# Optimization experiments

Hardware: AMD Instinct MI355X
Metric: run time of the kernel (lower is better)

The kernel has to match this reference:

```python
import jax, jax.numpy as jnp
import numpy as np
from jax import lax

K, N = 256, 65536

def setup_inputs() -> dict:
    key = jax.random.key(0)
    k1, k2, k3 = jax.random.split(key, 3)
    # obs: non-negative event counts [K, N]
    obs = jax.random.uniform(k1, (K, N), dtype=jnp.float32) * 4.0
    # Beta ~ U(1, 3) [K]
    Beta = 1.0 + 2.0 * jax.random.uniform(k2, (K,), dtype=jnp.float32)
    # Alpha ~ U(0, 0.01) [K, K]
    Alpha = 0.01 * jax.random.uniform(k3, (K, K), dtype=jnp.float32)
    return {"obs": obs, "Beta": Beta, "Alpha": Alpha}

def reference(obs, Beta, Alpha):
    # obs: [K, N], Beta: [K], Alpha: [K, K]
    Kk, Nn = obs.shape
    Mu0 = obs.mean(axis=1) / 10.0 + 0.01            # [K] background rate
    decay = jnp.exp(-Beta)                          # [K]

    # Exponential kernel sum S[t] = sum_{tp<t} obs[:,tp] * Beta * exp(-(t-tp)*Beta)
    # admits recursion H[t] = exp(-Beta) * (H[t-1] + obs[:, t-1]), S[t] = Beta * H[t]
    def step(h, o_prev):
        h_new = decay * (h + o_prev)
        return h_new, h_new

    _, H = lax.scan(step, jnp.zeros((Kk,), obs.dtype), obs[:, :Nn - 1].T)  # [N-1, K]
    S = H * Beta                                    # [N-1, K]
    # lam1[:, t] = softplus(Alpha @ S[t]) for t >= 1; lam1[:, 0] = 0 (by original code)
    lam = jax.nn.softplus(jnp.einsum('jk,tk->tj', Alpha, S))  # [N-1, K]
    lams1 = jnp.concatenate([jnp.zeros((Kk, 1), obs.dtype), lam.T], axis=1)  # [K, N]
    lams0 = jnp.broadcast_to(Mu0[:, None], (Kk, Nn))          # [K, N]

    Nloglams = obs * jnp.log(lams0 + lams1 + 1e-5)
    loglik = (Nloglams - lams0 - lams1).sum()
    return loglik, lams0, lams1
```

## Files before the change

### kernel.cpp

```cpp
#include <hip/hip_runtime.h>
#include <math.h>

#define KK 256
#define NN 65536
#define TT 128
#define TPAD 264
#define NB (NN / TT)

typedef __bf16 bf16x8 __attribute__((ext_vector_type(8)));
typedef float f32x4 __attribute__((ext_vector_type(4)));

__global__ __launch_bounds__(256) void alpha_kernel(const float* __restrict__ Alpha,
                                                    __bf16* __restrict__ AlphaB,
                                                    float* __restrict__ out) {
  const int i = blockIdx.x * 256 + threadIdx.x;
  AlphaB[i] = (__bf16)Alpha[i];
  if (i == 0) out[0] = 0.f;
}

__global__ __launch_bounds__(512, 4) void main_kernel(const float* __restrict__ obs,
                                                      const float* __restrict__ Beta,
                                                      const __bf16* __restrict__ AlphaB,
                                                      float* __restrict__ out,
                                                      float* __restrict__ P) {
  __shared__ __bf16 Slds[TT][TPAD];
  const int tid = threadIdx.x;
  const int bid = blockIdx.x;
  const int tb = ((bid & 7) << 6) | (bid >> 3);
  const int t0 = tb * TT;

  {
    const int ell = tid & 7;
    const int krow0 = tid >> 3;
    for (int it = 0; it < 4; ++it) {
      const int k = it * 64 + krow0;
      const float beta = Beta[k];
      const float d = expf(-beta);
      const float d2 = d * d, d4 = d2 * d2, d8 = d4 * d4;
      float dl = 1.f;
      if (ell & 1) dl *= d;
      if (ell & 2) dl *= d2;
      if (ell & 4) dl *= d4;
      const float* row = obs + (size_t)k * NN;
      float Hc = 0.f;
      if (t0 > 0) {
#pragma unroll
        for (int rnd = 0; rnd < 2; ++rnd) {
          const float u = row[t0 - 16 + rnd * 8 + ell];
          float X = u, y;
          y = __shfl_up(X, 1, 8); X += (ell >= 1 ? d  * y : 0.f);
          y = __shfl_up(X, 2, 8); X += (ell >= 2 ? d2 * y : 0.f);
          y = __shfl_up(X, 4, 8); X += (ell >= 4 ? d4 * y : 0.f);
          const float I7 = __shfl(X, 7, 8);
          Hc = d8 * Hc + d * I7;
        }
      }
      float rsum = 0.f;
#pragma unroll
      for (int rnd = 0; rnd < 16; ++rnd) {
        const int base = 8 * rnd;
        const float u = row[t0 + base + ell];
        rsum += u;
        float X = u, y;
        y = __shfl_up(X, 1, 8); X += (ell >= 1 ? d  * y : 0.f);
        y = __shfl_up(X, 2, 8); X += (ell >= 2 ? d2 * y : 0.f);
        y = __shfl_up(X, 4, 8); X += (ell >= 4 ? d4 * y : 0.f);
        const float Ip = __shfl_up(X, 1, 8);
        const float H = dl * Hc + (ell >= 1 ? d * Ip : 0.f);
        Slds[base + ell][k] = (__bf16)(beta * H);
        const float I7 = __shfl(X, 7, 8);
        Hc = d8 * Hc + d * I7;
      }
      rsum += __shfl_down(rsum, 1, 8);
      rsum += __shfl_down(rsum, 2, 8);
      rsum += __shfl_down(rsum, 4, 8);
      if (ell == 0) P[(size_t)tb * KK + k] = rsum;
    }
  }
  __syncthreads();

  const int wave = tid >> 6;
  const int wj = wave & 3, wc = wave >> 2;
  const int lane = tid & 63;
  const int lquad = lane >> 4;
  const int l16 = lane & 15;

  f32x4 acc[4][4];
#pragma unroll
  for (int a = 0; a < 4; ++a)
#pragma unroll
    for (int b = 0; b < 4; ++b) acc[a][b] = (f32x4){0.f, 0.f, 0.f, 0.f};

  const __bf16* Abase = AlphaB + (size_t)(wj * 64 + l16) * KK + lquad * 8;
  for (int k0 = 0; k0 < KK; k0 += 32) {
    bf16x8 afrag[4], bfrag[4];
#pragma unroll
    for (int js = 0; js < 4; ++js)
      afrag[js] = *(const bf16x8*)(Abase + (size_t)js * 16 * KK + k0);
#pragma unroll
    for (int ts = 0; ts < 4; ++ts)
      bfrag[ts] = *(const bf16x8*)&Slds[wc * 64 + ts * 16 + l16][k0 + lquad * 8];
#pragma unroll
    for (int js = 0; js < 4; ++js)
#pragma unroll
      for (int ts = 0; ts < 4; ++ts)
        acc[js][ts] = __builtin_amdgcn_mfma_f32_16x16x32_bf16(
            afrag[js], bfrag[ts], acc[js][ts], 0, 0, 0);
  }

  float* lams1 = out + 1 + (size_t)KK * NN;
  const int tcol = t0 + wc * 64;
#pragma unroll
  for (int js = 0; js < 4; ++js) {
#pragma unroll
    for (int r = 0; r < 4; ++r) {
      const int j = wj * 64 + js * 16 + lquad * 4 + r;
      const size_t rowoff = (size_t)j * NN + tcol + l16;
#pragma unroll
      for (int ts = 0; ts < 4; ++ts) {
        float v = acc[js][ts][r];
        float lam = v + __logf(1.f + __expf(-v));
        if (tcol + ts * 16 + l16 == 0) lam = 0.f;
        lams1[rowoff + ts * 16] = lam;
      }
    }
  }
}

__global__ __launch_bounds__(512) void loglik_kernel(const float* __restrict__ obs,
                                                     const float* __restrict__ P,
                                                     float* __restrict__ out) {
  const int j = blockIdx.x;
  const int tid = threadIdx.x;

  float s = P[(size_t)tid * KK + j];
  __shared__ float red[512];
  red[tid] = s;
  __syncthreads();
  for (int off = 256; off > 0; off >>= 1) {
    if (tid < off) red[tid] += red[tid + off];
    __syncthreads();
  }
  const float m = red[0] * (1.0f / NN) * 0.1f + 0.01f;

  const float* orow = obs + (size_t)j * NN;
  float* l0row = out + 1 + (size_t)j * NN;
  float* l1row = l0row + (size_t)KK * NN;
  float partial = 0.f;
#pragma unroll 8
  for (int i = 0; i < NN / 512; ++i) {
    const int t = tid + i * 512;
    const float l1 = l1row[t];
    const float o = orow[t];
    l0row[t] = m;
    partial += o * __logf(m + l1 + 1e-5f) - m - l1;
  }

#pragma unroll
  for (int off = 32; off > 0; off >>= 1)
    partial += __shfl_down(partial, off, 64);
  __syncthreads();
  if ((tid & 63) == 0) red[tid >> 6] = partial;
  __syncthreads();
  if (tid == 0) {
    float t = 0.f;
#pragma unroll
    for (int w = 0; w < 8; ++w) t += red[w];
    atomicAdd(out, t);
  }
}

extern "C" void kernel_launch(void* const* d_in, const int* in_sizes, int n_in,
                              void* d_out, int out_size, void* d_ws, size_t ws_size,
                              hipStream_t stream) {
  const float* obs   = (const float*)d_in[0];
  const float* Beta  = (const float*)d_in[1];
  const float* Alpha = (const float*)d_in[2];
  float* out = (float*)d_out;

  __bf16* AlphaB = (__bf16*)d_ws;
  float* P = (float*)(AlphaB + (size_t)KK * KK);

  hipLaunchKernelGGL(alpha_kernel, dim3(KK), dim3(256), 0, stream, Alpha, AlphaB, out);
  hipLaunchKernelGGL(main_kernel, dim3(NB), dim3(512), 0, stream,
                     obs, Beta, AlphaB, out, P);
  hipLaunchKernelGGL(loglik_kernel, dim3(KK), dim3(512), 0, stream, obs, P, out);
}
```

Baseline: 228.5 us.

## Fuse log-likelihood into GEMM epilogue and precompute Mu0 in a prep pass

A prep kernel now computes the per-row background rate Mu0 (a full read of obs) and also converts Alpha to bf16. The main kernel's epilogue then computes the log-likelihood term from the freshly computed lams1 and atomically accumulates it, so lams1 no longer has to be re-read from global memory. A separate lightweight kernel writes the broadcast lams0 with vectorized stores. This removes the second pass over lams1 and obs, at the cost of an extra obs read in the prep kernel and strided, partially uncoalesced obs loads in the epilogue.

```diff
diff --git a/kernel.cpp b/kernel.cpp
--- a/kernel.cpp
+++ b/kernel.cpp
@@ -10,24 +10,47 @@
 typedef __bf16 bf16x8 __attribute__((ext_vector_type(8)));
 typedef float f32x4 __attribute__((ext_vector_type(4)));
 
-__global__ __launch_bounds__(256) void alpha_kernel(const float* __restrict__ Alpha,
-                                                    __bf16* __restrict__ AlphaB,
-                                                    float* __restrict__ out) {
-  const int i = blockIdx.x * 256 + threadIdx.x;
-  AlphaB[i] = (__bf16)Alpha[i];
-  if (i == 0) out[0] = 0.f;
+__global__ __launch_bounds__(512) void prep_kernel(const float* __restrict__ obs,
+                                                   const float* __restrict__ Alpha,
+                                                   float* __restrict__ mu0,
+                                                   __bf16* __restrict__ AlphaB,
+                                                   float* __restrict__ out) {
+  const int j = blockIdx.x;
+  const int tid = threadIdx.x;
+  if (tid < KK) AlphaB[(size_t)j * KK + tid] = (__bf16)Alpha[(size_t)j * KK + tid];
+  const float4* p = (const float4*)(obs + (size_t)j * NN) + tid;
+  float s = 0.f;
+#pragma unroll
+  for (int i = 0; i < 32; ++i) {
+    float4 v = p[i * 512];
+    s += (v.x + v.y) + (v.z + v.w);
+  }
+  __shared__ float red[512];
+  red[tid] = s;
+  __syncthreads();
+  for (int off = 256; off > 0; off >>= 1) {
+    if (tid < off) red[tid] += red[tid + off];
+    __syncthreads();
+  }
+  if (tid == 0) {
+    mu0[j] = red[0] * (1.0f / NN) * 0.1f + 0.01f;
+    if (j == 0) out[0] = 0.f;
+  }
 }
 
 __global__ __launch_bounds__(512, 4) void main_kernel(const float* __restrict__ obs,
                                                       const float* __restrict__ Beta,
+                                                      const float* __restrict__ mu0,
                                                       const __bf16* __restrict__ AlphaB,
-                                                      float* __restrict__ out,
-                                                      float* __restrict__ P) {
+                                                      float* __restrict__ out) {
   __shared__ __bf16 Slds[TT][TPAD];
+  __shared__ float mu0s[KK];
   const int tid = threadIdx.x;
   const int bid = blockIdx.x;
   const int tb = ((bid & 7) << 6) | (bid >> 3);
   const int t0 = tb * TT;
+
+  if (tid < KK) mu0s[tid] = mu0[tid];
 
   {
     const int ell = tid & 7;
@@ -55,12 +78,10 @@
           Hc = d8 * Hc + d * I7;
         }
       }
-      float rsum = 0.f;
 #pragma unroll
       for (int rnd = 0; rnd < 16; ++rnd) {
         const int base = 8 * rnd;
         const float u = row[t0 + base + ell];
-        rsum += u;
         float X = u, y;
         y = __shfl_up(X, 1, 8); X += (ell >= 1 ? d  * y : 0.f);
         y = __shfl_up(X, 2, 8); X += (ell >= 2 ? d2 * y : 0.f);
@@ -71,10 +92,6 @@
         const float I7 = __shfl(X, 7, 8);
         Hc = d8 * Hc + d * I7;
       }
-      rsum += __shfl_down(rsum, 1, 8);
-      rsum += __shfl_down(rsum, 2, 8);
-      rsum += __shfl_down(rsum, 4, 8);
-      if (ell == 0) P[(size_t)tb * KK + k] = rsum;
     }
   }
   __syncthreads();
@@ -108,6 +125,7 @@
             afrag[js], bfrag[ts], acc[js][ts], 0, 0, 0);
   }
 
+  float partial = 0.f;
   float* lams1 = out + 1 + (size_t)KK * NN;
   const int tcol = t0 + wc * 64;
 #pragma unroll
@@ -115,6 +133,7 @@
 #pragma unroll
     for (int r = 0; r < 4; ++r) {
       const int j = wj * 64 + js * 16 + lquad * 4 + r;
+      const float m = mu0s[j];
       const size_t rowoff = (size_t)j * NN + tcol + l16;
 #pragma unroll
       for (int ts = 0; ts < 4; ++ts) {
@@ -122,45 +141,18 @@
         float lam = v + __logf(1.f + __expf(-v));
         if (tcol + ts * 16 + l16 == 0) lam = 0.f;
         lams1[rowoff + ts * 16] = lam;
+        const float o = obs[rowoff + ts * 16];
+        partial += o * __logf(m + lam + 1e-5f) - m - lam;
       }
     }
-  }
-}
-
-__global__ __launch_bounds__(512) void loglik_kernel(const float* __restrict__ obs,
-                                                     const float* __restrict__ P,
-                                                     float* __restrict__ out) {
-  const int j = blockIdx.x;
-  const int tid = threadIdx.x;
-
-  float s = P[(size_t)tid * KK + j];
-  __shared__ float red[512];
-  red[tid] = s;
-  __syncthreads();
-  for (int off = 256; off > 0; off >>= 1) {
-    if (tid < off) red[tid] += red[tid + off];
-    __syncthreads();
-  }
-  const float m = red[0] * (1.0f / NN) * 0.1f + 0.01f;
-
-  const float* orow = obs + (size_t)j * NN;
-  float* l0row = out + 1 + (size_t)j * NN;
-  float* l1row = l0row + (size_t)KK * NN;
-  float partial = 0.f;
-#pragma unroll 8
-  for (int i = 0; i < NN / 512; ++i) {
-    const int t = tid + i * 512;
-    const float l1 = l1row[t];
-    const float o = orow[t];
-    l0row[t] = m;
-    partial += o * __logf(m + l1 + 1e-5f) - m - l1;
   }
 
 #pragma unroll
   for (int off = 32; off > 0; off >>= 1)
     partial += __shfl_down(partial, off, 64);
   __syncthreads();
-  if ((tid & 63) == 0) red[tid >> 6] = partial;
+  float* red = (float*)&Slds[0][0];
+  if (lane == 0) red[wave] = partial;
   __syncthreads();
   if (tid == 0) {
     float t = 0.f;
@@ -168,6 +160,19 @@
     for (int w = 0; w < 8; ++w) t += red[w];
     atomicAdd(out, t);
   }
+}
+
+__global__ __launch_bounds__(512) void lams0_kernel(const float* __restrict__ mu0,
+                                                    float* __restrict__ out) {
+  const int j = blockIdx.x;
+  const int tid = threadIdx.x;
+  const float m = mu0[j];
+  float* row0 = out + 1 + (size_t)j * NN;
+  if (tid < 3) row0[tid] = m;
+  if (tid == 3) row0[NN - 1] = m;
+  f32x4* p4 = (f32x4*)(row0 + 3);
+  const f32x4 mv = {m, m, m, m};
+  for (int i = tid; i < (NN - 4) / 4; i += 512) p4[i] = mv;
 }
 
 extern "C" void kernel_launch(void* const* d_in, const int* in_sizes, int n_in,
@@ -179,10 +184,11 @@
   float* out = (float*)d_out;
 
   __bf16* AlphaB = (__bf16*)d_ws;
-  float* P = (float*)(AlphaB + (size_t)KK * KK);
+  float* mu0 = (float*)(AlphaB + (size_t)KK * KK);
 
-  hipLaunchKernelGGL(alpha_kernel, dim3(KK), dim3(256), 0, stream, Alpha, AlphaB, out);
+  hipLaunchKernelGGL(prep_kernel, dim3(KK), dim3(512), 0, stream, obs, Alpha,
+                     mu0, AlphaB, out);
   hipLaunchKernelGGL(main_kernel, dim3(NB), dim3(512), 0, stream,
-                     obs, Beta, AlphaB, out, P);
-  hipLaunchKernelGGL(loglik_kernel, dim3(KK), dim3(512), 0, stream, obs, P, out);
+                     obs, Beta, mu0, AlphaB, out);
+  hipLaunchKernelGGL(lams0_kernel, dim3(KK), dim3(512), 0, stream, mu0, out);
 }
```

Result: slower. 240.4 us (+5.2%).

## Double time tile, stage lams1 through LDS for coalesced vector stores

Applied to the files above, without the earlier changes.

Doubles the time tile to 256 steps with 1024-thread blocks, halving the number of blocks and their scan warm-up prefixes. The MFMA results are written through shared memory (reusing the S buffer) in two halves so each wave can emit contiguous 16-byte stores along rows of lams1, replacing the scattered 4-byte column stores. The per-block row-sum partials are stored transposed so the loglik kernel can read them contiguously. The trade-offs are extra barriers, fewer resident waves, and LDS traffic for the staging step.

```diff
diff --git a/kernel.cpp b/kernel.cpp
--- a/kernel.cpp
+++ b/kernel.cpp
@@ -3,8 +3,9 @@
 
 #define KK 256
 #define NN 65536
-#define TT 128
+#define TT 256
 #define TPAD 264
+#define CP 260
 #define NB (NN / TT)
 
 typedef __bf16 bf16x8 __attribute__((ext_vector_type(8)));
@@ -18,22 +19,22 @@
   if (i == 0) out[0] = 0.f;
 }
 
-__global__ __launch_bounds__(512, 4) void main_kernel(const float* __restrict__ obs,
-                                                      const float* __restrict__ Beta,
-                                                      const __bf16* __restrict__ AlphaB,
-                                                      float* __restrict__ out,
-                                                      float* __restrict__ P) {
-  __shared__ __bf16 Slds[TT][TPAD];
+__global__ __launch_bounds__(1024, 4) void main_kernel(const float* __restrict__ obs,
+                                                       const float* __restrict__ Beta,
+                                                       const __bf16* __restrict__ AlphaB,
+                                                       float* __restrict__ out,
+                                                       float* __restrict__ P) {
+  __shared__ __align__(16) __bf16 Slds[TT][TPAD];
   const int tid = threadIdx.x;
   const int bid = blockIdx.x;
-  const int tb = ((bid & 7) << 6) | (bid >> 3);
+  const int tb = ((bid & 7) << 5) | (bid >> 3);
   const int t0 = tb * TT;
 
   {
     const int ell = tid & 7;
     const int krow0 = tid >> 3;
-    for (int it = 0; it < 4; ++it) {
-      const int k = it * 64 + krow0;
+    for (int it = 0; it < 2; ++it) {
+      const int k = it * 128 + krow0;
       const float beta = Beta[k];
       const float d = expf(-beta);
       const float d2 = d * d, d4 = d2 * d2, d8 = d4 * d4;
@@ -57,7 +58,7 @@
       }
       float rsum = 0.f;
 #pragma unroll
-      for (int rnd = 0; rnd < 16; ++rnd) {
+      for (int rnd = 0; rnd < 32; ++rnd) {
         const int base = 8 * rnd;
         const float u = row[t0 + base + ell];
         rsum += u;
@@ -74,7 +75,7 @@
       rsum += __shfl_down(rsum, 1, 8);
       rsum += __shfl_down(rsum, 2, 8);
       rsum += __shfl_down(rsum, 4, 8);
-      if (ell == 0) P[(size_t)tb * KK + k] = rsum;
+      if (ell == 0) P[(size_t)k * NB + tb] = rsum;
     }
   }
   __syncthreads();
@@ -108,21 +109,35 @@
             afrag[js], bfrag[ts], acc[js][ts], 0, 0, 0);
   }
 
+  float* Cl = (float*)&Slds[0][0];
   float* lams1 = out + 1 + (size_t)KK * NN;
-  const int tcol = t0 + wc * 64;
-#pragma unroll
-  for (int js = 0; js < 4; ++js) {
-#pragma unroll
-    for (int r = 0; r < 4; ++r) {
-      const int j = wj * 64 + js * 16 + lquad * 4 + r;
-      const size_t rowoff = (size_t)j * NN + tcol + l16;
-#pragma unroll
-      for (int ts = 0; ts < 4; ++ts) {
-        float v = acc[js][ts][r];
-        float lam = v + __logf(1.f + __expf(-v));
-        if (tcol + ts * 16 + l16 == 0) lam = 0.f;
-        lams1[rowoff + ts * 16] = lam;
+#pragma unroll
+  for (int h = 0; h < 2; ++h) {
+    __syncthreads();
+    if ((wj >> 1) == h) {
+      const int jb = (wj & 1) * 64;
+#pragma unroll
+      for (int js = 0; js < 4; ++js) {
+#pragma unroll
+        for (int r = 0; r < 4; ++r) {
+          const int jr = jb + js * 16 + lquad * 4 + r;
+#pragma unroll
+          for (int ts = 0; ts < 4; ++ts) {
+            const int tr = wc * 64 + ts * 16 + l16;
+            float v = acc[js][ts][r];
+            float lam = v + __logf(1.f + __expf(-v));
+            if (t0 + tr == 0) lam = 0.f;
+            Cl[jr * CP + tr] = lam;
+          }
+        }
       }
+    }
+    __syncthreads();
+#pragma unroll
+    for (int rr = 0; rr < 8; ++rr) {
+      const int jr = wave * 8 + rr;
+      const f32x4 v = *(const f32x4*)&Cl[jr * CP + 4 * lane];
+      *(f32x4*)&lams1[(size_t)(h * 128 + jr) * NN + t0 + 4 * lane] = v;
     }
   }
 }
@@ -133,7 +148,7 @@
   const int j = blockIdx.x;
   const int tid = threadIdx.x;
 
-  float s = P[(size_t)tid * KK + j];
+  float s = (tid < NB) ? P[(size_t)j * NB + tid] : 0.f;
   __shared__ float red[512];
   red[tid] = s;
   __syncthreads();
@@ -182,7 +197,7 @@
   float* P = (float*)(AlphaB + (size_t)KK * KK);
 
   hipLaunchKernelGGL(alpha_kernel, dim3(KK), dim3(256), 0, stream, Alpha, AlphaB, out);
-  hipLaunchKernelGGL(main_kernel, dim3(NB), dim3(512), 0, stream,
+  hipLaunchKernelGGL(main_kernel, dim3(NB), dim3(1024), 0, stream,
                      obs, Beta, AlphaB, out, P);
   hipLaunchKernelGGL(loglik_kernel, dim3(KK), dim3(512), 0, stream, obs, P, out);
 }
```

Result: slower. 235.3 us (+3.0%).
